# Performance work log

Hardware: AMD Instinct MI355X
Metric: run time of the kernel (lower is better)

The kernel has to match this reference:

```python
import jax, jax.numpy as jnp
import numpy as np

B, S, D, MAX_LEN = 8, 2048, 512, 2048
NEG_INF = jnp.float32(-jnp.inf)


def setup_inputs() -> dict:
    key = jax.random.key(0)
    ks = jax.random.split(key, 10)
    s = 1.0 / np.sqrt(D)
    inp = {
        "x": jax.random.normal(ks[0], (B, S, D), dtype=jnp.float32),
        "pos_table": jax.random.normal(ks[1], (MAX_LEN, D), dtype=jnp.float32) * 0.02,
        "Wq": jax.random.normal(ks[2], (D, D), dtype=jnp.float32) * s,
        "bq": jnp.zeros((D,), dtype=jnp.float32),
        "Wk": jax.random.normal(ks[3], (D, D), dtype=jnp.float32) * s,
        "bk": jnp.zeros((D,), dtype=jnp.float32),
        "Wv": jax.random.normal(ks[4], (D, D), dtype=jnp.float32) * s,
        "bv": jnp.zeros((D,), dtype=jnp.float32),
        "Wd": jax.random.normal(ks[5], (D, D), dtype=jnp.float32) * s,
        "bd": jnp.zeros((D,), dtype=jnp.float32),
    }
    return inp


def reference(x, pos_table, Wq, bq, Wk, bk, Wv, bv, Wd, bd):
    # add learned positional embeddings (add_pos=True path): arange over seq dim
    x = x + pos_table[:x.shape[-2]]  # [B,S,D]
    # torch nn.Linear: y = x @ W.T + b
    q = jnp.einsum("bsd,ed->bse", x, Wq) + bq
    k = jnp.einsum("bsd,ed->bse", x, Wk) + bk
    v = jnp.einsum("bsd,ed->bse", x, Wv) + bv
    v = jnp.where(jnp.isnan(v), 0.0, v)  # nan_to_num(nan=0)
    scale = 1.0 / jnp.sqrt(jnp.float32(D))
    scores = jnp.einsum("bqd,bkd->bqk", q, k) * scale  # [B,S,S]
    scores = jnp.where(jnp.isnan(scores), NEG_INF, scores)  # nan_to_num(nan=-inf)
    attn = jax.nn.softmax(scores, axis=2)
    y = jnp.einsum("bqk,bkd->bqd", attn, v)
    return jnp.einsum("bsd,ed->bse", y, Wd) + bd
```

## Files before the change

kernel.cpp:

```cpp
#include <hip/hip_runtime.h>
#include <stdint.h>

typedef __bf16 bf16x8 __attribute__((ext_vector_type(8)));
typedef float f32x4 __attribute__((ext_vector_type(4)));

static constexpr float QK_SCALE = 0.044194173824159216f;

__device__ __forceinline__ uint16_t f2bf(float f) {
    uint32_t x = __builtin_bit_cast(uint32_t, f);
    x += 0x7FFFu + ((x >> 16) & 1u);
    return (uint16_t)(x >> 16);
}

__device__ __forceinline__ void cp16(const uint16_t* g, uint16_t* l) {
    __builtin_amdgcn_global_load_lds(
        (__attribute__((address_space(1))) void*)(uint16_t*)g,
        (__attribute__((address_space(3))) void*)l,
        16, 0, 0);
}

template <int MODE>
__global__ __launch_bounds__(256, 3) void gemm_nt(
    const uint16_t* __restrict__ A, const uint16_t* __restrict__ Bm,
    void* __restrict__ C0, void* __restrict__ C1, void* __restrict__ C2,
    const float* __restrict__ bias0, const float* __restrict__ bias1,
    const float* __restrict__ bias2,
    float scale, int K, int ldc, long bsA, long bsB, long bsC,
    int scols, int stPerBatch)
{
    __shared__ __align__(16) uint16_t SH[3][8192];

    const uint32_t id  = blockIdx.x;
    const uint32_t xcd = id & 7u;
    const uint32_t p   = id >> 3;
    const uint32_t q   = p >> 4;
    const uint32_t w   = p & 15u;
    const uint32_t g   = q * 8u + xcd;
    const uint32_t bz  = g / (uint32_t)stPerBatch;
    const uint32_t gs  = g - bz * (uint32_t)stPerBatch;
    const uint32_t sr  = gs / (uint32_t)scols;
    const uint32_t sc  = gs - sr * (uint32_t)scols;
    const int bm = (int)(sr * 4u + (w >> 2));
    const int bn = (int)(sc * 4u + (w & 3u));

    const int t  = threadIdx.x;
    const int wave = t >> 6, lane = t & 63;
    const int wm = (wave >> 1) * 64, wn = (wave & 1) * 64;
    const int lm = lane & 15, lq = lane >> 4;
    const int sw = lq ^ ((lm >> 1) & 3);

    const uint16_t* Ab = A  + (long)bz * bsA + (long)bm * 128 * K;
    const uint16_t* Bb = Bm + (long)bz * bsB + (long)bn * 128 * K;

    long goff[2]; int loff[2];
#pragma unroll
    for (int j = 0; j < 2; ++j) {
        const int s  = j * 256 + t;
        const int r  = s >> 2;
        const int cs = s & 3;
        const int cg = cs ^ ((r >> 1) & 3);
        goff[j] = (long)r * K + cg * 8;
        loff[j] = s * 8;
    }

    const int KI = K >> 5;

#pragma unroll
    for (int st = 0; st < 2; ++st)
#pragma unroll
        for (int j = 0; j < 2; ++j) {
            cp16(Ab + goff[j] + st * 32, SH[st] + loff[j]);
            cp16(Bb + goff[j] + st * 32, SH[st] + 4096 + loff[j]);
        }

    f32x4 acc[4][4] = {};

    int cur = 0, pf = 2;
    for (int k = 0; k < KI; ++k) {
        asm volatile("s_waitcnt vmcnt(4) lgkmcnt(0)\n\ts_barrier" ::: "memory");

        int kp = k + 2; if (kp >= KI) kp = KI - 1;
        uint16_t* dst = SH[pf];
        const long ko = (long)kp * 32;
#pragma unroll
        for (int j = 0; j < 2; ++j) {
            cp16(Ab + goff[j] + ko, dst + loff[j]);
            cp16(Bb + goff[j] + ko, dst + 4096 + loff[j]);
        }

        const uint16_t* buf = SH[cur];
        bf16x8 af[4], bfr[4];
#pragma unroll
        for (int i = 0; i < 4; ++i)
            af[i]  = *(const bf16x8*)&buf[((wm + i * 16 + lm) * 4 + sw) * 8];
#pragma unroll
        for (int i = 0; i < 4; ++i)
            bfr[i] = *(const bf16x8*)&buf[4096 + ((wn + i * 16 + lm) * 4 + sw) * 8];

#pragma unroll
        for (int i = 0; i < 4; ++i)
#pragma unroll
            for (int j = 0; j < 4; ++j)
                acc[i][j] = __builtin_amdgcn_mfma_f32_16x16x32_bf16(
                    bfr[i], af[j], acc[i][j], 0, 0, 0);

        cur = (cur == 2) ? 0 : cur + 1;
        pf  = (pf  == 2) ? 0 : pf  + 1;
    }

    const int mb = bm * 128 + wm + lm;
    const int nb = bn * 128 + wn + lq * 4;
    if (MODE == 0) {
#pragma unroll
        for (int j = 0; j < 4; ++j) {
            const int m = mb + j * 16;
#pragma unroll
            for (int i = 0; i < 4; ++i) {
                const int n = nb + i * 16;
                const uint32_t lo = (uint32_t)f2bf(acc[i][j][0] * scale) |
                                    ((uint32_t)f2bf(acc[i][j][1] * scale) << 16);
                const uint32_t hi = (uint32_t)f2bf(acc[i][j][2] * scale) |
                                    ((uint32_t)f2bf(acc[i][j][3] * scale) << 16);
                *(uint2*)&((uint16_t*)C0)[(long)bz * bsC + (long)m * ldc + n] =
                    make_uint2(lo, hi);
            }
        }
        return;
    }
    if (MODE == 7) {
#pragma unroll
        for (int j = 0; j < 4; ++j) {
            const int m = mb + j * 16;
            const float inv = 1.f / bias1[m];
#pragma unroll
            for (int i = 0; i < 4; ++i) {
                const int n = nb + i * 16;
                const float4 b4 = *(const float4*)&bias0[n];
                *(float4*)&((float*)C0)[(long)m * ldc + n] = make_float4(
                    acc[i][j][0] * inv + b4.x, acc[i][j][1] * inv + b4.y,
                    acc[i][j][2] * inv + b4.z, acc[i][j][3] * inv + b4.w);
            }
        }
        return;
    }
#pragma unroll
    for (int i = 0; i < 4; ++i) {
        const int n = nb + i * 16;
        const int sec = n >> 9, nn = n & 511;
        const float* bp = sec == 0 ? bias0 : (sec == 1 ? bias1 : bias2);
        const float4 b4 = *(const float4*)&bp[nn];
#pragma unroll
        for (int j = 0; j < 4; ++j) {
            const int m = mb + j * 16;
            if (sec < 2) {
                uint16_t* Cq = (uint16_t*)(sec == 0 ? C0 : C1);
                const uint32_t lo = (uint32_t)f2bf(acc[i][j][0] + b4.x) |
                                    ((uint32_t)f2bf(acc[i][j][1] + b4.y) << 16);
                const uint32_t hi = (uint32_t)f2bf(acc[i][j][2] + b4.z) |
                                    ((uint32_t)f2bf(acc[i][j][3] + b4.w) << 16);
                *(uint2*)&Cq[(long)m * 512 + nn] = make_uint2(lo, hi);
            } else {
                const int bb = m >> 11, ss = m & 2047;
                uint16_t* vt = (uint16_t*)C2 + ((long)bb * 512 + nn) * 2048 + ss;
                vt[0]        = f2bf(acc[i][j][0] + b4.x);
                vt[2048]     = f2bf(acc[i][j][1] + b4.y);
                vt[2 * 2048] = f2bf(acc[i][j][2] + b4.z);
                vt[3 * 2048] = f2bf(acc[i][j][3] + b4.w);
            }
        }
    }
}

template <int MODE>
__global__ __launch_bounds__(512, 2) void gemm_nt8(
    const uint16_t* __restrict__ A, const uint16_t* __restrict__ Bm,
    void* __restrict__ C0, float* __restrict__ rowsum,
    float scale, int K, int ldc, long bsA, long bsB, long bsC,
    int scols, int stPerBatch)
{
    __shared__ __align__(16) uint16_t SH[3][16384];

    const uint32_t id  = blockIdx.x;
    const uint32_t xcd = id & 7u;
    const uint32_t p   = id >> 3;
    const uint32_t q   = p >> 4;
    const uint32_t w   = p & 15u;
    const uint32_t g   = q * 8u + xcd;
    const uint32_t bz  = g / (uint32_t)stPerBatch;
    const uint32_t gs  = g - bz * (uint32_t)stPerBatch;
    const uint32_t sr  = gs / (uint32_t)scols;
    const uint32_t sc  = gs - sr * (uint32_t)scols;
    const int bm = (int)(sr * 4u + (w >> 2));
    const int bn = (int)(sc * 4u + (w & 3u));

    const int t  = threadIdx.x;
    const int wave = t >> 6, lane = t & 63;
    const int wm2 = (wave >> 2) * 128;
    const int wn2 = (wave & 3) * 64;
    const int lm = lane & 15, lq = lane >> 4;
    const int sw = lq ^ ((lm >> 1) & 3);

    const uint16_t* Ab = A  + (long)bz * bsA + (long)bm * 256 * K;
    const uint16_t* Bb = Bm + (long)bz * bsB + (long)bn * 256 * K;

    long goff[2]; int loff[2];
#pragma unroll
    for (int j = 0; j < 2; ++j) {
        const int s  = j * 512 + t;
        const int r  = s >> 2;
        const int cs = s & 3;
        const int cg = cs ^ ((r >> 1) & 3);
        goff[j] = (long)r * K + cg * 8;
        loff[j] = s * 8;
    }

    const int KI = K >> 5;

#pragma unroll
    for (int st = 0; st < 2; ++st)
#pragma unroll
        for (int j = 0; j < 2; ++j) {
            cp16(Ab + goff[j] + st * 32, SH[st] + loff[j]);
            cp16(Bb + goff[j] + st * 32, SH[st] + 8192 + loff[j]);
        }

    f32x4 acc[4][8] = {};

    int cur = 0, pf = 2;
    for (int k = 0; k < KI; ++k) {
        asm volatile("s_waitcnt vmcnt(4) lgkmcnt(0)\n\ts_barrier" ::: "memory");

        int kp = k + 2; if (kp >= KI) kp = KI - 1;
        uint16_t* dst = SH[pf];
        const long ko = (long)kp * 32;
#pragma unroll
        for (int j = 0; j < 2; ++j) {
            cp16(Ab + goff[j] + ko, dst + loff[j]);
            cp16(Bb + goff[j] + ko, dst + 8192 + loff[j]);
        }

        const uint16_t* buf = SH[cur];
        bf16x8 af[8], bfr[4];
#define RDA(jj) (*(const bf16x8*)&buf[((wm2 + (jj) * 16 + lm) * 4 + sw) * 8])
#define RDB(ii) (*(const bf16x8*)&buf[8192 + ((wn2 + (ii) * 16 + lm) * 4 + sw) * 8])
        bfr[0] = RDB(0); bfr[1] = RDB(1); bfr[2] = RDB(2); bfr[3] = RDB(3);
        af[0] = RDA(0); af[1] = RDA(1); af[2] = RDA(2); af[3] = RDA(3);
        af[4] = RDA(4); af[5] = RDA(5); af[6] = RDA(6); af[7] = RDA(7);
#pragma unroll
        for (int pp = 0; pp < 4; ++pp) {
            __builtin_amdgcn_s_setprio(1);
#pragma unroll
            for (int i = 0; i < 4; ++i) {
                acc[i][2 * pp]     = __builtin_amdgcn_mfma_f32_16x16x32_bf16(
                    bfr[i], af[2 * pp],     acc[i][2 * pp],     0, 0, 0);
                acc[i][2 * pp + 1] = __builtin_amdgcn_mfma_f32_16x16x32_bf16(
                    bfr[i], af[2 * pp + 1], acc[i][2 * pp + 1], 0, 0, 0);
            }
            __builtin_amdgcn_s_setprio(0);
        }
#undef RDA
#undef RDB

        cur = (cur == 2) ? 0 : cur + 1;
        pf  = (pf  == 2) ? 0 : pf  + 1;
    }

    const int mb = bm * 256 + wm2 + lm;
    const int nb = bn * 256 + wn2 + lq * 4;
#pragma unroll
    for (int j = 0; j < 8; ++j) {
        const int m = mb + j * 16;
        float rsj = 0.f;
#pragma unroll
        for (int i = 0; i < 4; ++i) {
            const int n = nb + i * 16;
            const float v0 = __expf(acc[i][j][0] * scale);
            const float v1 = __expf(acc[i][j][1] * scale);
            const float v2 = __expf(acc[i][j][2] * scale);
            const float v3 = __expf(acc[i][j][3] * scale);
            rsj += (v0 + v1) + (v2 + v3);
            const uint32_t lo = (uint32_t)f2bf(v0) | ((uint32_t)f2bf(v1) << 16);
            const uint32_t hi = (uint32_t)f2bf(v2) | ((uint32_t)f2bf(v3) << 16);
            *(uint2*)&((uint16_t*)C0)[(long)bz * bsC + (long)m * ldc + n] =
                make_uint2(lo, hi);
        }
        rsj += __shfl_xor(rsj, 16);
        rsj += __shfl_xor(rsj, 32);
        if (lq == 0)
            atomicAdd(&rowsum[(long)bz * 2048 + m], rsj);
    }
}

__global__ __launch_bounds__(256) void prep_x(const float* __restrict__ x,
                                              const float* __restrict__ pos,
                                              uint16_t* __restrict__ xb)
{
    const long i8 = ((long)blockIdx.x * 256 + threadIdx.x) * 8;
    const long p8 = i8 & ((1l << 20) - 1);
    const float4* xv = (const float4*)(x + i8);
    const float4* pv = (const float4*)(pos + p8);
    const float4 a0 = xv[0], a1 = xv[1];
    const float4 b0 = pv[0], b1 = pv[1];
    uint16_t o[8];
    o[0] = f2bf(a0.x + b0.x); o[1] = f2bf(a0.y + b0.y);
    o[2] = f2bf(a0.z + b0.z); o[3] = f2bf(a0.w + b0.w);
    o[4] = f2bf(a1.x + b1.x); o[5] = f2bf(a1.y + b1.y);
    o[6] = f2bf(a1.z + b1.z); o[7] = f2bf(a1.w + b1.w);
    *(uint4*)(xb + i8) = *(uint4*)o;
}

__global__ __launch_bounds__(256) void prep_w(
    const float* __restrict__ Wq, const float* __restrict__ Wk,
    const float* __restrict__ Wv, const float* __restrict__ Wd,
    uint16_t* __restrict__ wqkv, uint16_t* __restrict__ wd)
{
    const long f = ((long)blockIdx.x * 256 + threadIdx.x) * 8;
    const int  w = (int)(f >> 18);
    const long off = f & 262143;
    const float* src = (w == 0) ? Wq : (w == 1) ? Wk : (w == 2) ? Wv : Wd;
    uint16_t* dst = (w < 3) ? (wqkv + (long)w * 262144 + off) : (wd + off);
    const float4* s4 = (const float4*)(src + off);
    const float4 a = s4[0], b = s4[1];
    uint16_t o[8];
    o[0] = f2bf(a.x); o[1] = f2bf(a.y); o[2] = f2bf(a.z); o[3] = f2bf(a.w);
    o[4] = f2bf(b.x); o[5] = f2bf(b.y); o[6] = f2bf(b.z); o[7] = f2bf(b.w);
    *(uint4*)dst = *(uint4*)o;
}

extern "C" void kernel_launch(void* const* d_in, const int* in_sizes, int n_in,
                              void* d_out, int out_size, void* d_ws, size_t ws_size,
                              hipStream_t stream)
{
    const float* x   = (const float*)d_in[0];
    const float* pos = (const float*)d_in[1];
    const float* Wq  = (const float*)d_in[2];
    const float* bq  = (const float*)d_in[3];
    const float* Wk  = (const float*)d_in[4];
    const float* bk  = (const float*)d_in[5];
    const float* Wv  = (const float*)d_in[6];
    const float* bv  = (const float*)d_in[7];
    const float* Wd  = (const float*)d_in[8];
    const float* bd  = (const float*)d_in[9];
    float* out = (float*)d_out;

    char* ws = (char*)d_ws;
    uint16_t* xb   = (uint16_t*)(ws);
    uint16_t* wqkv = (uint16_t*)(ws + 16777216);
    uint16_t* wd   = (uint16_t*)(ws + 18350080);
    uint16_t* Qb   = (uint16_t*)(ws + 18874368);
    uint16_t* Kb   = (uint16_t*)(ws + 35651584);
    uint16_t* Vt   = (uint16_t*)(ws + 52428800);
    uint16_t* Pb   = (uint16_t*)(ws + 69206016);
    uint16_t* yb   = (uint16_t*)(ws + 136314880);
    float* rowsum = (float*)ws;

    prep_x<<<4096, 256, 0, stream>>>(x, pos, xb);
    prep_w<<<512, 256, 0, stream>>>(Wq, Wk, Wv, Wd, wqkv, wd);

    gemm_nt<3><<<1536, 256, 0, stream>>>(
        xb, wqkv, Qb, Kb, Vt, bq, bk, bv, 1.0f, 512, 512, 0, 0, 0, 3, 96);

    hipMemsetAsync(rowsum, 0, 16384 * sizeof(float), stream);

    gemm_nt8<4><<<512, 512, 0, stream>>>(
        Qb, Kb, Pb, rowsum, QK_SCALE, 512, 2048, (long)2048 * 512,
        (long)2048 * 512, (long)2048 * 2048, 2, 4);

    gemm_nt<0><<<512, 256, 0, stream>>>(
        Pb, Vt, yb, nullptr, nullptr, nullptr, nullptr, nullptr,
        1.0f, 2048, 512, (long)2048 * 2048, (long)512 * 2048,
        (long)2048 * 512, 1, 4);

    gemm_nt<7><<<512, 256, 0, stream>>>(
        yb, wd, out, nullptr, nullptr, bd, rowsum, nullptr,
        1.0f, 512, 512, 0, 0, 0, 1, 32);
}
```

Before: 267.4 us.

## Restructure QK^T GEMM main loop into fine-grained ping-pong phases

Replaces the 3-stage, 32-wide K loop of the QK^T score kernel with a 2-buffer scheme over 64-wide K tiles, where each tile is split into half-tiles. Each half-tile is processed in two phases, each loading a quarter of the A fragments, issuing one slice of the next global-to-LDS copies and running 16 MFMAs between barriers. The goal is to interleave LDS reads, async copies and MFMA work more finely, hiding memory latency and cutting register pressure from 8 A fragments to 4. In exchange it adds many more barriers per K step and relies on subtle vmcnt accounting for correctness.

After: 267.9 us. About the same (+0.2%).

```diff
diff --git a/kernel.cpp b/kernel.cpp
--- a/kernel.cpp
+++ b/kernel.cpp
@@ -171,14 +171,13 @@
     }
 }
 
-template <int MODE>
-__global__ __launch_bounds__(512, 2) void gemm_nt8(
+__global__ __launch_bounds__(512, 2) void gemm_qk8(
     const uint16_t* __restrict__ A, const uint16_t* __restrict__ Bm,
-    void* __restrict__ C0, float* __restrict__ rowsum,
+    uint16_t* __restrict__ C0, float* __restrict__ rowsum,
     float scale, int K, int ldc, long bsA, long bsB, long bsC,
     int scols, int stPerBatch)
 {
-    __shared__ __align__(16) uint16_t SH[3][16384];
+    __shared__ __align__(16) uint16_t SH[2][4][8192];
 
     const uint32_t id  = blockIdx.x;
     const uint32_t xcd = id & 7u;
@@ -214,56 +213,66 @@
         loff[j] = s * 8;
     }
 
-    const int KI = K >> 5;
-
-#pragma unroll
-    for (int st = 0; st < 2; ++st)
-#pragma unroll
-        for (int j = 0; j < 2; ++j) {
-            cp16(Ab + goff[j] + st * 32, SH[st] + loff[j]);
-            cp16(Bb + goff[j] + st * 32, SH[st] + 8192 + loff[j]);
-        }
+    const int TT = K >> 6;
+
+#define STG(src, tt, hh, dreg) do {                                            \
+    const long o_ = (long)(tt) * 64 + (hh) * 32;                               \
+    cp16((src) + goff[0] + o_, (dreg) + loff[0]);                              \
+    cp16((src) + goff[1] + o_, (dreg) + loff[1]); } while (0)
+
+    STG(Ab, 0, 0, SH[0][0]); STG(Bb, 0, 0, SH[0][2]);
+    STG(Ab, 0, 1, SH[0][1]); STG(Bb, 0, 1, SH[0][3]);
+    STG(Ab, 1, 0, SH[1][0]); STG(Bb, 1, 0, SH[1][2]);
+    asm volatile("s_waitcnt vmcnt(4)\n\ts_barrier" ::: "memory");
 
     f32x4 acc[4][8] = {};
-
-    int cur = 0, pf = 2;
-    for (int k = 0; k < KI; ++k) {
-        asm volatile("s_waitcnt vmcnt(4) lgkmcnt(0)\n\ts_barrier" ::: "memory");
-
-        int kp = k + 2; if (kp >= KI) kp = KI - 1;
-        uint16_t* dst = SH[pf];
-        const long ko = (long)kp * 32;
-#pragma unroll
-        for (int j = 0; j < 2; ++j) {
-            cp16(Ab + goff[j] + ko, dst + loff[j]);
-            cp16(Bb + goff[j] + ko, dst + 8192 + loff[j]);
-        }
-
-        const uint16_t* buf = SH[cur];
-        bf16x8 af[8], bfr[4];
-#define RDA(jj) (*(const bf16x8*)&buf[((wm2 + (jj) * 16 + lm) * 4 + sw) * 8])
-#define RDB(ii) (*(const bf16x8*)&buf[8192 + ((wn2 + (ii) * 16 + lm) * 4 + sw) * 8])
-        bfr[0] = RDB(0); bfr[1] = RDB(1); bfr[2] = RDB(2); bfr[3] = RDB(3);
-        af[0] = RDA(0); af[1] = RDA(1); af[2] = RDA(2); af[3] = RDA(3);
-        af[4] = RDA(4); af[5] = RDA(5); af[6] = RDA(6); af[7] = RDA(7);
-#pragma unroll
-        for (int pp = 0; pp < 4; ++pp) {
-            __builtin_amdgcn_s_setprio(1);
-#pragma unroll
-            for (int i = 0; i < 4; ++i) {
-                acc[i][2 * pp]     = __builtin_amdgcn_mfma_f32_16x16x32_bf16(
-                    bfr[i], af[2 * pp],     acc[i][2 * pp],     0, 0, 0);
-                acc[i][2 * pp + 1] = __builtin_amdgcn_mfma_f32_16x16x32_bf16(
-                    bfr[i], af[2 * pp + 1], acc[i][2 * pp + 1], 0, 0, 0);
-            }
-            __builtin_amdgcn_s_setprio(0);
-        }
-#undef RDA
-#undef RDB
-
-        cur = (cur == 2) ? 0 : cur + 1;
-        pf  = (pf  == 2) ? 0 : pf  + 1;
-    }
+    bf16x8 af[4], bfr[4];
+
+#define RDA_(bb, hh, jj) (*(const bf16x8*)&SH[bb][hh]                          \
+    [((wm2 + (jj) * 16 + lm) * 4 + sw) * 8])
+#define RDB_(bb, hh, ii) (*(const bf16x8*)&SH[bb][2 + (hh)]                    \
+    [((wn2 + (ii) * 16 + lm) * 4 + sw) * 8])
+#define VMC4 asm volatile("s_waitcnt vmcnt(4)" ::: "memory")
+#define PHASE(bb, hh, gg, STAGE_STMT, GUARD)                                   \
+    if ((gg) == 0) {                                                           \
+        bfr[0] = RDB_(bb, hh, 0); bfr[1] = RDB_(bb, hh, 1);                    \
+        bfr[2] = RDB_(bb, hh, 2); bfr[3] = RDB_(bb, hh, 3);                    \
+    }                                                                          \
+    af[0] = RDA_(bb, hh, (gg) * 4 + 0); af[1] = RDA_(bb, hh, (gg) * 4 + 1);    \
+    af[2] = RDA_(bb, hh, (gg) * 4 + 2); af[3] = RDA_(bb, hh, (gg) * 4 + 3);    \
+    STAGE_STMT;                                                                \
+    asm volatile("s_barrier" ::: "memory");                                    \
+    __builtin_amdgcn_s_setprio(1);                                             \
+    _Pragma("unroll")                                                          \
+    for (int i_ = 0; i_ < 4; ++i_) {                                           \
+        _Pragma("unroll")                                                      \
+        for (int j_ = 0; j_ < 4; ++j_)                                         \
+            acc[i_][(gg) * 4 + j_] = __builtin_amdgcn_mfma_f32_16x16x32_bf16(  \
+                bfr[i_], af[j_], acc[i_][(gg) * 4 + j_], 0, 0, 0);             \
+    }                                                                          \
+    __builtin_amdgcn_s_setprio(0);                                             \
+    GUARD;                                                                     \
+    asm volatile("s_barrier" ::: "memory");
+
+    const int NI = TT >> 1;
+    for (int it = 0; it < NI; ++it) {
+        const int t1 = 2 * it + 1;
+        const int u2 = (2 * it + 2 < TT) ? 2 * it + 2 : TT - 1;
+        const int u3 = (2 * it + 3 < TT) ? 2 * it + 3 : TT - 1;
+        PHASE(0, 0, 0, STG(Ab, t1, 1, SH[1][1]), )
+        PHASE(0, 0, 1, STG(Bb, t1, 1, SH[1][3]), )
+        PHASE(0, 1, 0, STG(Ab, u2, 0, SH[0][0]), )
+        PHASE(0, 1, 1, STG(Bb, u2, 0, SH[0][2]), VMC4)
+        PHASE(1, 0, 0, STG(Ab, u2, 1, SH[0][1]), )
+        PHASE(1, 0, 1, STG(Bb, u2, 1, SH[0][3]), )
+        PHASE(1, 1, 0, STG(Ab, u3, 0, SH[1][0]), )
+        PHASE(1, 1, 1, STG(Bb, u3, 0, SH[1][2]), VMC4)
+    }
+#undef PHASE
+#undef VMC4
+#undef RDA_
+#undef RDB_
+#undef STG
 
     const int mb = bm * 256 + wm2 + lm;
     const int nb = bn * 256 + wn2 + lq * 4;
@@ -281,7 +290,7 @@
             rsj += (v0 + v1) + (v2 + v3);
             const uint32_t lo = (uint32_t)f2bf(v0) | ((uint32_t)f2bf(v1) << 16);
             const uint32_t hi = (uint32_t)f2bf(v2) | ((uint32_t)f2bf(v3) << 16);
-            *(uint2*)&((uint16_t*)C0)[(long)bz * bsC + (long)m * ldc + n] =
+            *(uint2*)&C0[(long)bz * bsC + (long)m * ldc + n] =
                 make_uint2(lo, hi);
         }
         rsj += __shfl_xor(rsj, 16);
@@ -362,7 +371,7 @@
 
     hipMemsetAsync(rowsum, 0, 16384 * sizeof(float), stream);
 
-    gemm_nt8<4><<<512, 512, 0, stream>>>(
+    gemm_qk8<<<512, 512, 0, stream>>>(
         Qb, Kb, Pb, rowsum, QK_SCALE, 512, 2048, (long)2048 * 512,
         (long)2048 * 512, (long)2048 * 2048, 2, 4);
 
```
